# Kernel tuning notes

Hardware: AMD Instinct MI355X
Metric: run time of the kernel (lower is better)

Reference implementation:

```python
import jax, jax.numpy as jnp
import numpy as np

NUM_HEAD = 16
MASKED_BIAS = -10000.0


def setup_inputs() -> dict:
    key = jax.random.key(0)
    k1, k2, k3 = jax.random.split(key, 3)
    B, M, N = 2, 2048, 1024
    x = jax.random.normal(k1, (B, M, N), dtype=jnp.float32)
    w_attn = jax.random.normal(k2, (N, 3 * N), dtype=jnp.float32) * 0.02
    w_proj = jax.random.normal(k3, (N, N), dtype=jnp.float32) * 0.02
    b_attn = jnp.zeros((3 * N,), dtype=jnp.float32)
    b_proj = jnp.zeros((N,), dtype=jnp.float32)
    return {"x": x, "w_attn": w_attn, "w_proj": w_proj,
            "b_attn": b_attn, "b_proj": b_proj}


def reference(x, w_attn, w_proj, b_attn, b_proj):
    B, M, N = x.shape
    H = NUM_HEAD
    d = N // H  # head dim
    # fused QKV projection: [B,M,3N]
    qkv = jnp.einsum('bmn,nd->bmd', x, w_attn) + b_attn
    q, k, v = jnp.split(qkv, 3, axis=-1)
    # split heads -> [B,H,M,d]
    q = q.reshape(B, M, H, d).transpose(0, 2, 1, 3)
    k = k.reshape(B, M, H, d).transpose(0, 2, 1, 3)
    v = v.reshape(B, M, H, d).transpose(0, 2, 1, 3)
    # scaled dot-product scores [B,H,M,M]
    scores = jnp.einsum('bhqd,bhkd->bhqk', q, k) / jnp.sqrt(jnp.float32(d))
    causal = jnp.tril(jnp.ones((M, M), dtype=bool))  # GPT-2 bias buffer
    scores = jnp.where(causal, scores, jnp.float32(MASKED_BIAS))
    attn = jax.nn.softmax(scores, axis=-1)
    # context [B,H,M,d] -> [B,M,N]
    ctx = jnp.einsum('bhqk,bhkd->bhqd', attn, v)
    ctx = ctx.transpose(0, 2, 1, 3).reshape(B, M, N)
    # output projection
    out = jnp.einsum('bmn,no->bmo', ctx, w_proj) + b_proj
    return out
```

## Files before the change

### kernel.cpp

```cpp
#include <hip/hip_runtime.h>

typedef __attribute__((ext_vector_type(8))) __bf16 bf16x8;
typedef __attribute__((ext_vector_type(4))) float f32x4;

__device__ __forceinline__ void async_copy16(const void* g, void* l) {
    __builtin_amdgcn_global_load_lds(
        (const __attribute__((address_space(1))) void*)g,
        (__attribute__((address_space(3))) void*)l, 16, 0, 0);
}

__global__ __launch_bounds__(256) void cast_bf16_k(
    const float* __restrict__ src, __bf16* __restrict__ dst)
{
    size_t i = ((size_t)blockIdx.x * 256 + threadIdx.x) * 8;
    float4 a = *(const float4*)&src[i];
    float4 b = *(const float4*)&src[i + 4];
    bf16x8 o;
    o[0] = (__bf16)a.x; o[1] = (__bf16)a.y; o[2] = (__bf16)a.z; o[3] = (__bf16)a.w;
    o[4] = (__bf16)b.x; o[5] = (__bf16)b.y; o[6] = (__bf16)b.z; o[7] = (__bf16)b.w;
    *(bf16x8*)&dst[i] = o;
}

__global__ __launch_bounds__(256) void transpose_cast_k(
    const float* __restrict__ src, __bf16* __restrict__ dst, int R, int C)
{
    __shared__ float tile[32][33];
    int c0 = blockIdx.x * 32, r0 = blockIdx.y * 32;
    int tx = threadIdx.x & 31, ty = threadIdx.x >> 5;
    for (int i = ty; i < 32; i += 8)
        tile[i][tx] = src[(size_t)(r0 + i) * C + (c0 + tx)];
    __syncthreads();
    for (int i = ty; i < 32; i += 8)
        dst[(size_t)(c0 + i) * R + (r0 + tx)] = (__bf16)tile[tx][i];
}

template <int MODE>
__global__ __launch_bounds__(256) void gemm_bt(
    const __bf16* __restrict__ A, const __bf16* __restrict__ Bt,
    const float* __restrict__ bias, int K,
    __bf16* __restrict__ O0, __bf16* __restrict__ O1, __bf16* __restrict__ O2,
    float* __restrict__ Of)
{
    __shared__ __align__(16) __bf16 lds_a[128 * 32];
    __shared__ __align__(16) __bf16 lds_b[128 * 32];
    const int row0 = blockIdx.x * 128;
    const int col0 = blockIdx.y * 128;
    const int tid  = threadIdx.x;
    const int lane = tid & 63;
    const int w    = tid >> 6;
    const int wm   = (w >> 1) * 64, wn = (w & 1) * 64;
    const int quad = lane >> 4, l16 = lane & 15;
    const int rsw  = (quad ^ (l16 & 3)) * 8;

    f32x4 acc[4][4] = {};
    for (int kb = 0; kb < K; kb += 32) {
#pragma unroll
        for (int t = 0; t < 2; ++t) {
            int c = t * 64 + lane;
            int row = 32 * w + (c >> 2);
            int gch = (c & 3) ^ (row & 3);
            async_copy16(&A[(size_t)(row0 + row) * K + kb + gch * 8],
                         (char*)lds_a + (w * 128 + t * 64) * 16);
            async_copy16(&Bt[(size_t)(col0 + row) * K + kb + gch * 8],
                         (char*)lds_b + (w * 128 + t * 64) * 16);
        }
        __syncthreads();
        bf16x8 af[4], bfr[4];
#pragma unroll
        for (int i = 0; i < 4; ++i)
            af[i] = *(const bf16x8*)&lds_a[(wm + i * 16 + l16) * 32 + rsw];
#pragma unroll
        for (int j = 0; j < 4; ++j)
            bfr[j] = *(const bf16x8*)&lds_b[(wn + j * 16 + l16) * 32 + rsw];
#pragma unroll
        for (int i = 0; i < 4; ++i)
#pragma unroll
            for (int j = 0; j < 4; ++j)
                acc[i][j] = __builtin_amdgcn_mfma_f32_16x16x32_bf16(
                    af[i], bfr[j], acc[i][j], 0, 0, 0);
        __syncthreads();
    }

#pragma unroll
    for (int i = 0; i < 4; ++i) {
        int grow = row0 + wm + i * 16 + quad * 4;
#pragma unroll
        for (int j = 0; j < 4; ++j) {
            int gcol = col0 + wn + j * 16 + l16;
            float bv = bias[gcol];
            if constexpr (MODE == 0) {
                int which = gcol >> 10;
                int n  = gcol & 1023;
                int hh = n >> 6, dd = n & 63;
#pragma unroll
                for (int r = 0; r < 4; ++r) {
                    int gr = grow + r;
                    int bb = gr >> 11, mm = gr & 2047;
                    int bhh = bb * 16 + hh;
                    float v = acc[i][j][r] + bv;
                    if (which == 0)
                        O0[((size_t)bhh * 2048 + mm) * 64 + dd] =
                            (__bf16)(v * 0.18033688011112042f);
                    else if (which == 1)
                        O1[((size_t)bhh * 2048 + mm) * 64 + dd] = (__bf16)v;
                    else
                        O2[((size_t)bhh * 64 + dd) * 2048 + mm] = (__bf16)v;
                }
            } else {
#pragma unroll
                for (int r = 0; r < 4; ++r) {
                    int gr = grow + r;
                    Of[(size_t)gr * 1024 + gcol] = acc[i][j][r] + bv;
                }
            }
        }
    }
}

__global__ __launch_bounds__(256) void attn_kernel(
    const __bf16* __restrict__ Qh, const __bf16* __restrict__ Kh,
    const __bf16* __restrict__ Vt, __bf16* __restrict__ ctx)
{
    const int M = 2048, D = 64;
    const int bh = blockIdx.x;
    const int qt = 31 - blockIdx.y;
    const int b = bh >> 4, h = bh & 15;
    const int tid = threadIdx.x, lane = tid & 63, w = tid >> 6;
    const int quad = lane >> 4, l16 = lane & 15;

    const int q0 = qt * 64;
    const int nIter = qt + 1;

    __shared__ __align__(16) __bf16 lds_k[2][64 * 64];
    __shared__ __align__(16) __bf16 lds_v[2][64 * 64];
    __shared__ __align__(16) __bf16 lds_p[4][16 * 72];

    const __bf16* Qp = Qh + (size_t)bh * M * D;
    const __bf16* Kp = Kh + (size_t)bh * M * D;
    const __bf16* Vp = Vt + (size_t)bh * D * M;

    const int qbase = q0 + w * 16;

    bf16x8 qf[2];
#pragma unroll
    for (int c = 0; c < 2; ++c)
        qf[c] = *(const bf16x8*)
            &Qp[(size_t)(qbase + l16) * D + c * 32 + quad * 8];

    f32x4 acc[4] = {};
    f32x4 acc_s = {};
    const __bf16 onev = (__bf16)1.0f;
    const bf16x8 ones = {onev, onev, onev, onev, onev, onev, onev, onev};

    auto stage = [&](int pb, int kb) {
#pragma unroll
        for (int t = 0; t < 2; ++t) {
            int c = w * 128 + t * 64 + lane;
            int row = c >> 3, ch = c & 7;
            int gch = ch ^ (row & 7);
            async_copy16(&Kp[(size_t)(kb + row) * 64 + gch * 8],
                         (char*)&lds_k[pb][0] + (w * 128 + t * 64) * 16);
            async_copy16(&Vp[(size_t)row * M + kb + gch * 8],
                         (char*)&lds_v[pb][0] + (w * 128 + t * 64) * 16);
        }
    };

    stage(0, 0);
    __bf16* pl = &lds_p[w][0];

    for (int it = 0; it < nIter; ++it) {
        const int kb = it << 6;
        __syncthreads();
        if (it + 1 < nIter) stage((it + 1) & 1, kb + 64);
        const __bf16* kt = &lds_k[it & 1][0];
        const __bf16* vt = &lds_v[it & 1][0];

        f32x4 s[4];
#pragma unroll
        for (int j = 0; j < 4; ++j) {
            f32x4 t = {};
#pragma unroll
            for (int c = 0; c < 2; ++c) {
                int ch = ((c << 2) + quad) ^ (l16 & 7);
                bf16x8 kf = *(const bf16x8*)
                    &kt[(((j << 4) + l16) << 6) + (ch << 3)];
                t = __builtin_amdgcn_mfma_f32_16x16x32_bf16(
                    qf[c], kf, t, 0, 0, 0);
            }
            s[j] = t;
        }
        if (kb + 63 > qbase) {
#pragma unroll
            for (int j = 0; j < 4; ++j)
#pragma unroll
                for (int r = 0; r < 4; ++r)
                    if (kb + j * 16 + l16 > qbase + quad * 4 + r)
                        s[j][r] = -1e30f;
        }
#pragma unroll
        for (int j = 0; j < 4; ++j)
#pragma unroll
            for (int r = 0; r < 4; ++r)
                s[j][r] = exp2f(s[j][r]);
#pragma unroll
        for (int j = 0; j < 4; ++j)
#pragma unroll
            for (int r = 0; r < 4; ++r)
                pl[(quad * 4 + r) * 72 + j * 16 + l16] = (__bf16)s[j][r];
        bf16x8 pf[2];
#pragma unroll
        for (int c = 0; c < 2; ++c)
            pf[c] = *(const bf16x8*)&pl[l16 * 72 + c * 32 + quad * 8];
#pragma unroll
        for (int f = 0; f < 4; ++f)
#pragma unroll
            for (int c = 0; c < 2; ++c) {
                int ch = ((c << 2) + quad) ^ (l16 & 7);
                bf16x8 vf = *(const bf16x8*)
                    &vt[(((f << 4) + l16) << 6) + (ch << 3)];
                acc[f] = __builtin_amdgcn_mfma_f32_16x16x32_bf16(
                    pf[c], vf, acc[f], 0, 0, 0);
            }
#pragma unroll
        for (int c = 0; c < 2; ++c)
            acc_s = __builtin_amdgcn_mfma_f32_16x16x32_bf16(
                pf[c], ones, acc_s, 0, 0, 0);
    }

#pragma unroll
    for (int f = 0; f < 4; ++f)
#pragma unroll
        for (int r = 0; r < 4; ++r) {
            int q = qbase + quad * 4 + r;
            int col = h * 64 + f * 16 + l16;
            ctx[((size_t)(b * 2048 + q)) * 1024 + col] =
                (__bf16)(acc[f][r] / acc_s[r]);
        }
}

extern "C" void kernel_launch(void* const* d_in, const int* in_sizes, int n_in,
                              void* d_out, int out_size, void* d_ws, size_t ws_size,
                              hipStream_t stream) {
    const float* x      = (const float*)d_in[0];
    const float* w_attn = (const float*)d_in[1];
    const float* w_proj = (const float*)d_in[2];
    const float* b_attn = (const float*)d_in[3];
    const float* b_proj = (const float*)d_in[4];
    float* out = (float*)d_out;

    char* ws = (char*)d_ws;
    __bf16* xb  = (__bf16*)(ws);
    __bf16* ctx = (__bf16*)(ws);
    __bf16* wAt = (__bf16*)(ws + 8388608);
    __bf16* wPt = (__bf16*)(ws + 14680064);
    __bf16* Vt  = (__bf16*)(ws + 16777216);
    __bf16* Qh  = (__bf16*)d_out;
    __bf16* Kh  = (__bf16*)d_out + 4194304;

    cast_bf16_k<<<2048, 256, 0, stream>>>(x, xb);
    transpose_cast_k<<<dim3(96, 32), 256, 0, stream>>>(w_attn, wAt, 1024, 3072);
    transpose_cast_k<<<dim3(32, 32), 256, 0, stream>>>(w_proj, wPt, 1024, 1024);
    gemm_bt<0><<<dim3(32, 24), 256, 0, stream>>>(xb, wAt, b_attn, 1024,
                                                 Qh, Kh, Vt, nullptr);
    attn_kernel<<<dim3(32, 32), 256, 0, stream>>>(Qh, Kh, Vt, ctx);
    gemm_bt<1><<<dim3(32, 8), 256, 0, stream>>>(ctx, wPt, b_proj, 1024,
                                                nullptr, nullptr, nullptr, out);
}
```

Baseline: 201.3 us.

## Rework GEMM LDS swizzle, vectorize V-transpose stores, narrow proj tile

Changes the GEMM LDS layout so each 128-byte line holds two rows with an XOR swizzle over 8 chunks, meant to cut LDS bank conflicts on fragment reads. The V output, stored transposed, now goes out as packed 4-element bf16 stores instead of scalar stores. The output-projection GEMM is templated to a 64-wide N tile, giving 512 blocks instead of 256 for better CU occupancy, at the cost of less B reuse per block.

```diff
diff --git a/kernel.cpp b/kernel.cpp
--- a/kernel.cpp
+++ b/kernel.cpp
@@ -1,6 +1,7 @@
 #include <hip/hip_runtime.h>
 
 typedef __attribute__((ext_vector_type(8))) __bf16 bf16x8;
+typedef __attribute__((ext_vector_type(4))) __bf16 bf16x4;
 typedef __attribute__((ext_vector_type(4))) float f32x4;
 
 __device__ __forceinline__ void async_copy16(const void* g, void* l) {
@@ -34,48 +35,60 @@
         dst[(size_t)(c0 + i) * R + (r0 + tx)] = (__bf16)tile[tx][i];
 }
 
-template <int MODE>
+template <int MODE, int TN>
 __global__ __launch_bounds__(256) void gemm_bt(
     const __bf16* __restrict__ A, const __bf16* __restrict__ Bt,
     const float* __restrict__ bias, int K,
     __bf16* __restrict__ O0, __bf16* __restrict__ O1, __bf16* __restrict__ O2,
     float* __restrict__ Of)
 {
+    constexpr int NJ = TN / 32;
     __shared__ __align__(16) __bf16 lds_a[128 * 32];
-    __shared__ __align__(16) __bf16 lds_b[128 * 32];
+    __shared__ __align__(16) __bf16 lds_b[TN * 32];
     const int row0 = blockIdx.x * 128;
-    const int col0 = blockIdx.y * 128;
+    const int col0 = blockIdx.y * TN;
     const int tid  = threadIdx.x;
     const int lane = tid & 63;
     const int w    = tid >> 6;
-    const int wm   = (w >> 1) * 64, wn = (w & 1) * 64;
+    const int wm   = (w >> 1) * 64, wn = (w & 1) * (TN / 2);
     const int quad = lane >> 4, l16 = lane & 15;
-    const int rsw  = (quad ^ (l16 & 3)) * 8;
-
-    f32x4 acc[4][4] = {};
+
+    f32x4 acc[4][NJ] = {};
     for (int kb = 0; kb < K; kb += 32) {
 #pragma unroll
         for (int t = 0; t < 2; ++t) {
-            int c = t * 64 + lane;
-            int row = 32 * w + (c >> 2);
-            int gch = (c & 3) ^ (row & 3);
-            async_copy16(&A[(size_t)(row0 + row) * K + kb + gch * 8],
-                         (char*)lds_a + (w * 128 + t * 64) * 16);
-            async_copy16(&Bt[(size_t)(col0 + row) * K + kb + gch * 8],
-                         (char*)lds_b + (w * 128 + t * 64) * 16);
+            int s = t * 256 + tid;
+            int L = s >> 3, c = (s & 7) ^ (L & 7);
+            int row = 2 * L + (c >> 2), ch = c & 3;
+            async_copy16(&A[(size_t)(row0 + row) * K + kb + ch * 8],
+                         (char*)lds_a + (t * 256 + w * 64) * 16);
+        }
+#pragma unroll
+        for (int t = 0; t < TN / 64; ++t) {
+            int s = t * 256 + tid;
+            int L = s >> 3, c = (s & 7) ^ (L & 7);
+            int row = 2 * L + (c >> 2), ch = c & 3;
+            async_copy16(&Bt[(size_t)(col0 + row) * K + kb + ch * 8],
+                         (char*)lds_b + (t * 256 + w * 64) * 16);
         }
         __syncthreads();
-        bf16x8 af[4], bfr[4];
+        bf16x8 af[4], bfr[NJ];
+#pragma unroll
+        for (int i = 0; i < 4; ++i) {
+            int r = wm + i * 16 + l16;
+            int L = r >> 1, g = ((r & 1) * 4 + quad) ^ (L & 7);
+            af[i] = *(const bf16x8*)&lds_a[L * 64 + g * 8];
+        }
+#pragma unroll
+        for (int j = 0; j < NJ; ++j) {
+            int r = wn + j * 16 + l16;
+            int L = r >> 1, g = ((r & 1) * 4 + quad) ^ (L & 7);
+            bfr[j] = *(const bf16x8*)&lds_b[L * 64 + g * 8];
+        }
 #pragma unroll
         for (int i = 0; i < 4; ++i)
-            af[i] = *(const bf16x8*)&lds_a[(wm + i * 16 + l16) * 32 + rsw];
-#pragma unroll
-        for (int j = 0; j < 4; ++j)
-            bfr[j] = *(const bf16x8*)&lds_b[(wn + j * 16 + l16) * 32 + rsw];
-#pragma unroll
-        for (int i = 0; i < 4; ++i)
-#pragma unroll
-            for (int j = 0; j < 4; ++j)
+#pragma unroll
+            for (int j = 0; j < NJ; ++j)
                 acc[i][j] = __builtin_amdgcn_mfma_f32_16x16x32_bf16(
                     af[i], bfr[j], acc[i][j], 0, 0, 0);
         __syncthreads();
@@ -85,26 +98,32 @@
     for (int i = 0; i < 4; ++i) {
         int grow = row0 + wm + i * 16 + quad * 4;
 #pragma unroll
-        for (int j = 0; j < 4; ++j) {
+        for (int j = 0; j < NJ; ++j) {
             int gcol = col0 + wn + j * 16 + l16;
             float bv = bias[gcol];
             if constexpr (MODE == 0) {
                 int which = gcol >> 10;
                 int n  = gcol & 1023;
                 int hh = n >> 6, dd = n & 63;
-#pragma unroll
-                for (int r = 0; r < 4; ++r) {
-                    int gr = grow + r;
-                    int bb = gr >> 11, mm = gr & 2047;
-                    int bhh = bb * 16 + hh;
-                    float v = acc[i][j][r] + bv;
-                    if (which == 0)
-                        O0[((size_t)bhh * 2048 + mm) * 64 + dd] =
-                            (__bf16)(v * 0.18033688011112042f);
-                    else if (which == 1)
-                        O1[((size_t)bhh * 2048 + mm) * 64 + dd] = (__bf16)v;
-                    else
-                        O2[((size_t)bhh * 64 + dd) * 2048 + mm] = (__bf16)v;
+                int bb = grow >> 11, mm0 = grow & 2047;
+                int bhh = bb * 16 + hh;
+                if (which == 2) {
+                    bf16x4 pk;
+#pragma unroll
+                    for (int r = 0; r < 4; ++r)
+                        pk[r] = (__bf16)(acc[i][j][r] + bv);
+                    *(bf16x4*)&O2[((size_t)bhh * 64 + dd) * 2048 + mm0] = pk;
+                } else {
+#pragma unroll
+                    for (int r = 0; r < 4; ++r) {
+                        float v = acc[i][j][r] + bv;
+                        if (which == 0)
+                            O0[((size_t)bhh * 2048 + mm0 + r) * 64 + dd] =
+                                (__bf16)(v * 0.18033688011112042f);
+                        else
+                            O1[((size_t)bhh * 2048 + mm0 + r) * 64 + dd] =
+                                (__bf16)v;
+                    }
                 }
             } else {
 #pragma unroll
@@ -260,9 +279,9 @@
     cast_bf16_k<<<2048, 256, 0, stream>>>(x, xb);
     transpose_cast_k<<<dim3(96, 32), 256, 0, stream>>>(w_attn, wAt, 1024, 3072);
     transpose_cast_k<<<dim3(32, 32), 256, 0, stream>>>(w_proj, wPt, 1024, 1024);
-    gemm_bt<0><<<dim3(32, 24), 256, 0, stream>>>(xb, wAt, b_attn, 1024,
-                                                 Qh, Kh, Vt, nullptr);
+    gemm_bt<0, 128><<<dim3(32, 24), 256, 0, stream>>>(xb, wAt, b_attn, 1024,
+                                                      Qh, Kh, Vt, nullptr);
     attn_kernel<<<dim3(32, 32), 256, 0, stream>>>(Qh, Kh, Vt, ctx);
-    gemm_bt<1><<<dim3(32, 8), 256, 0, stream>>>(ctx, wPt, b_proj, 1024,
-                                                nullptr, nullptr, nullptr, out);
-}
+    gemm_bt<1, 64><<<dim3(32, 16), 256, 0, stream>>>(ctx, wPt, b_proj, 1024,
+                                                     nullptr, nullptr, nullptr, out);
+}
```

Measured after the change: 188.1 us. -6.6%, faster.
